# Performance work log

Hardware: AMD Instinct MI355X
Metric: run time of the kernel (lower is better)

## Reference

```python
import jax, jax.numpy as jnp
import numpy as np

N = 25000        # nodes
E = 400000       # edges (avg degree 16)
F_IN = 256       # input node feature dim
C = 32           # tensor-product channels (linear_1 output)
A = 9            # spherical-harmonic dim (lmax=2)
WNUM = C * A     # per-edge TP weight numel (_head_weight_numel)
B = 8            # radial basis size (edge embedding)
H = 64           # edge MLP hidden width
S = 4            # species (node_attrs one-hot width)
F_OUT = 256      # output node feature dim
AVG_NEIGH = 16.0


def setup_inputs() -> dict:
    key = jax.random.key(0)
    ks = jax.random.split(key, 11)
    sc = lambda fan: np.float32(1.0 / np.sqrt(fan))
    return {
        "x": jax.random.normal(ks[0], (N, F_IN), jnp.float32),
        "node_attrs": jax.random.uniform(ks[1], (N, S), jnp.float32),
        "edge_embedding": jax.random.uniform(ks[2], (E, B), jnp.float32),
        "edge_attr": jax.random.normal(ks[3], (E, A), jnp.float32),
        "edge_index": jax.random.randint(ks[4], (2, E), 0, N, jnp.int32),
        "W1": jax.random.normal(ks[5], (F_IN, C), jnp.float32) * sc(F_IN),
        "Wm1": jax.random.normal(ks[6], (B, H), jnp.float32) * sc(B),
        "Wm2": jax.random.normal(ks[7], (H, H), jnp.float32) * sc(H),
        "Wm3": jax.random.normal(ks[8], (H, WNUM), jnp.float32) * sc(H),
        "W2": jax.random.normal(ks[9], (WNUM, F_OUT), jnp.float32) * sc(WNUM),
        "Wsc": jax.random.normal(ks[10], (F_IN, S, F_OUT), jnp.float32) * sc(F_IN * S),
    }


def reference(x, node_attrs, edge_embedding, edge_attr, edge_index,
              W1, Wm1, Wm2, Wm3, W2, Wsc):
    # self-connection: FullyConnectedTensorProduct(x, node_attrs) -> [N, F_OUT]
    sc_out = jnp.einsum('nf,ns,fso->no', x, node_attrs, Wsc)

    # linear_1 + avg-neighbor normalization -> [N, C]
    h = (x @ W1) * (1.0 / jnp.sqrt(jnp.asarray(AVG_NEIGH, x.dtype)))

    # edge MLP on radial embedding -> per-edge TP weights [E, C, A]
    w = jax.nn.silu(edge_embedding @ Wm1)
    w = jax.nn.silu(w @ Wm2)
    w = (w @ Wm3).reshape(E, C, A)

    edge_dst = edge_index[0]
    edge_src = edge_index[1]

    # gather-TP-scatter: msg[e,c,a] = w[e,c,a] * h[src[e],c] * sh[e,a]
    msg = w * h[edge_src][:, :, None] * edge_attr[:, None, :]   # [E, C, A]
    agg = jax.ops.segment_sum(msg.reshape(E, WNUM), edge_dst,
                              num_segments=N)                    # [N, C*A]

    # linear_2 + activation + self-connection
    out = jax.nn.silu(agg @ W2) + sc_out                         # [N, F_OUT]
    return out
```

## Files before the change

kernel.cpp:

```cpp
#include <hip/hip_runtime.h>

#define NN   25000
#define EE   400000
#define FIN  256
#define CC   32
#define AA   9
#define WN   288
#define BB   8
#define HH   64
#define SS   4
#define FOUT 256
#define EPB  32

typedef float f32x4 __attribute__((ext_vector_type(4)));
typedef short short8 __attribute__((ext_vector_type(8)));

__device__ __forceinline__ float silu_f(float v){ return v / (1.0f + __expf(-v)); }

__device__ __forceinline__ unsigned short f2bf(float f){
  unsigned int u = __builtin_bit_cast(unsigned int, f);
  u += 0x7FFFu + ((u >> 16) & 1u);
  return (unsigned short)(u >> 16);
}

__global__ __launch_bounds__(256) void k_h(const float* __restrict__ x,
                                           const float* __restrict__ W1,
                                           float* __restrict__ h){
  int gid = blockIdx.x * 256 + threadIdx.x;
  int n = gid >> 5, c = gid & 31;
  const float* xr = x + (size_t)n * FIN;
  float acc = 0.f;
  #pragma unroll 8
  for (int f = 0; f < FIN; ++f) acc = fmaf(xr[f], W1[f * CC + c], acc);
  h[gid] = acc * 0.25f;
}

__global__ __launch_bounds__(256) void k_cvt(const float* __restrict__ Wm1,
                                             const float* __restrict__ Wm2,
                                             const float* __restrict__ Wm3,
                                             unsigned short* __restrict__ wm1t,
                                             unsigned short* __restrict__ wm2t,
                                             unsigned short* __restrict__ wm3t){
  int i = blockIdx.x * 256 + threadIdx.x;
  if (i < HH * 32){
    int n = i >> 5, k = i & 31;
    wm1t[i] = (k < BB) ? f2bf(Wm1[k * HH + n]) : (unsigned short)0;
  }
  if (i < HH * HH){
    int n = i >> 6, k = i & 63;
    wm2t[n * 64 + k] = f2bf(Wm2[k * HH + n]);
  }
  if (i < WN * HH){
    int n = i >> 6, k = i & 63;
    wm3t[n * 64 + k] = f2bf(Wm3[k * WN + n]);
  }
}

__global__ __launch_bounds__(256) void k_cvtsc(const float* __restrict__ Wsc,
                                               unsigned short* __restrict__ wscb){
  __shared__ float tile[32][33];
  const int k0 = blockIdx.x * 32;
  const int n0 = blockIdx.y * 32;
  const int t = threadIdx.x;
  #pragma unroll
  for (int p = 0; p < 4; ++p){
    int idx = t + p * 256;
    int r = idx >> 5, c = idx & 31;
    tile[r][c] = Wsc[(size_t)(k0 + r) * 256 + n0 + c];
  }
  __syncthreads();
  #pragma unroll
  for (int p = 0; p < 4; ++p){
    int idx = t + p * 256;
    int r = idx >> 5, c = idx & 31;
    wscb[(size_t)(n0 + r) * 1024 + k0 + c] = f2bf(tile[c][r]);
  }
}

__global__ __launch_bounds__(256) void k_hist(const int* __restrict__ eidx,
                                              int* __restrict__ cnt){
  int e = blockIdx.x * 256 + threadIdx.x;
  if (e < EE) atomicAdd(&cnt[eidx[e]], 1);
}

__global__ __launch_bounds__(1024) void k_scan(const int* __restrict__ cnt,
                                               int* __restrict__ cur){
  __shared__ int part[1024];
  const int t = threadIdx.x;
  const int base = t * 25;
  int s = 0;
  for (int i = 0; i < 25; ++i){
    int idx = base + i;
    s += (idx < NN) ? cnt[idx] : 0;
  }
  part[t] = s;
  __syncthreads();
  for (int off = 1; off < 1024; off <<= 1){
    int v = (t >= off) ? part[t - off] : 0;
    __syncthreads();
    part[t] += v;
    __syncthreads();
  }
  int run = part[t] - s;
  for (int i = 0; i < 25; ++i){
    int idx = base + i;
    if (idx < NN){
      cur[idx] = run;
      run += cnt[idx];
    }
  }
}

__global__ __launch_bounds__(256) void k_scatter(const int* __restrict__ eidx,
                                                 const float* __restrict__ eemb,
                                                 const float* __restrict__ sh,
                                                 int* __restrict__ cur,
                                                 unsigned short* __restrict__ ee_p,
                                                 float* __restrict__ sh_p,
                                                 int* __restrict__ src_p,
                                                 int* __restrict__ dst_p){
  int e = blockIdx.x * 256 + threadIdx.x;
  if (e < EE){
    int d = eidx[e];
    int p = atomicAdd(&cur[d], 1);
    dst_p[p] = d;
    src_p[p] = eidx[EE + e];
    float4 v0 = *(const float4*)&eemb[(size_t)e * BB];
    float4 v1 = *(const float4*)&eemb[(size_t)e * BB + 4];
    unsigned short t[8] = {f2bf(v0.x), f2bf(v0.y), f2bf(v0.z), f2bf(v0.w),
                           f2bf(v1.x), f2bf(v1.y), f2bf(v1.z), f2bf(v1.w)};
    *(short8*)&ee_p[(size_t)p * BB] = *(short8*)t;
    #pragma unroll
    for (int a = 0; a < AA; ++a) sh_p[(size_t)p * AA + a] = sh[(size_t)e * AA + a];
  }
}

__global__ __launch_bounds__(256) void k_sc(const float* __restrict__ x,
                                            const float* __restrict__ na,
                                            const unsigned short* __restrict__ wscb,
                                            float* __restrict__ out){
  __shared__ __align__(16) unsigned short As[64][72];
  __shared__ __align__(16) unsigned short Bs[256][72];
  const int tid = threadIdx.x;
  const int m0 = blockIdx.x * 64;
  const int sm = tid >> 2;
  const int sq = tid & 3;
  float4 nav = {0.f, 0.f, 0.f, 0.f};
  if (m0 + sm < NN) nav = *(const float4*)&na[(size_t)(m0 + sm) * SS];
  const float nf[4] = {nav.x, nav.y, nav.z, nav.w};
  const int lane = tid & 63, wv = tid >> 6;
  const int row = lane & 15, kg = lane >> 4;
  const f32x4 zf = {0.f, 0.f, 0.f, 0.f};
  f32x4 acc[16];
  #pragma unroll
  for (int i = 0; i < 16; ++i) acc[i] = zf;

  for (int kc = 0; kc < FIN * SS; kc += 64){
    __syncthreads();
    {
      float4 xv = {0.f, 0.f, 0.f, 0.f};
      int fc4 = (kc >> 2) + sq * 4;
      if (m0 + sm < NN) xv = *(const float4*)&x[(size_t)(m0 + sm) * FIN + fc4];
      float xf[4] = {xv.x, xv.y, xv.z, xv.w};
      unsigned short tmp[16];
      #pragma unroll
      for (int f = 0; f < 4; ++f)
        #pragma unroll
        for (int s = 0; s < 4; ++s) tmp[f * 4 + s] = f2bf(xf[f] * nf[s]);
      *(short8*)&As[sm][sq * 16]     = *(short8*)&tmp[0];
      *(short8*)&As[sm][sq * 16 + 8] = *(short8*)&tmp[8];
    }
    #pragma unroll
    for (int r = 0; r < 4; ++r){
      int ch = tid + r * 256;
      int n = ch >> 2, c4 = ch & 3;
      const unsigned short* src = wscb + (size_t)n * 1024 + kc + c4 * 16;
      *(short8*)&Bs[n][c4 * 16]     = *(const short8*)src;
      *(short8*)&Bs[n][c4 * 16 + 8] = *(const short8*)(src + 8);
    }
    __syncthreads();
    #pragma unroll
    for (int ks = 0; ks < 2; ++ks){
      short8 af = *(const short8*)&As[wv * 16 + row][ks * 32 + kg * 8];
      #pragma unroll
      for (int nt = 0; nt < 16; ++nt){
        short8 bfr = *(const short8*)&Bs[nt * 16 + row][ks * 32 + kg * 8];
        acc[nt] = __builtin_amdgcn_mfma_f32_16x16x32_bf16(af, bfr, acc[nt], 0, 0, 0);
      }
    }
  }
  #pragma unroll
  for (int nt = 0; nt < 16; ++nt){
    #pragma unroll
    for (int r = 0; r < 4; ++r){
      int m = m0 + wv * 16 + kg * 4 + r;
      if (m < NN) out[(size_t)m * FOUT + nt * 16 + row] = acc[nt][r];
    }
  }
}

__global__ __launch_bounds__(128) void k_edge(const unsigned short* __restrict__ ee_p,
                                              const float* __restrict__ sh_p,
                                              const int* __restrict__ src_p,
                                              const int* __restrict__ dst_p,
                                              const float* __restrict__ h,
                                              const unsigned short* __restrict__ wm1t,
                                              const unsigned short* __restrict__ wm2t,
                                              const unsigned short* __restrict__ wm3t,
                                              float* __restrict__ agg){
  __shared__ float sh_s[EPB][13];
  __shared__ float hs_s[EPB][36];
  __shared__ __align__(16) unsigned short t1b[EPB][72];
  __shared__ __align__(16) unsigned short t2b[EPB][72];
  const int tid = threadIdx.x;

  const int nwg = EE / EPB;
  const int q = nwg >> 3, rr = nwg & 7;
  int bid = blockIdx.x;
  int xcd = bid & 7, li = bid >> 3;
  int swz = (xcd < rr ? xcd * (q + 1) : rr * (q + 1) + (xcd - rr) * q) + li;
  const int e0 = swz * EPB;

  {
    int e = tid >> 2, c0 = (tid & 3) * 8;
    const float* hr = h + (size_t)src_p[e0 + e] * CC + c0;
    *(float4*)&hs_s[e][c0]     = *(const float4*)hr;
    *(float4*)&hs_s[e][c0 + 4] = *(const float4*)(hr + 4);
  }
  for (int i = tid; i < EPB * AA; i += 128){
    int e = i / 9, a = i - e * 9;
    sh_s[e][a] = sh_p[(size_t)e0 * AA + i];
  }
  __syncthreads();

  const int lane = tid & 63;
  const int wv   = tid >> 6;
  const int row  = lane & 15;
  const int kg   = lane >> 4;
  const f32x4 zf = {0.f, 0.f, 0.f, 0.f};

  {
    short8 a1 = {0, 0, 0, 0, 0, 0, 0, 0};
    if (kg == 0) a1 = *(const short8*)&ee_p[(size_t)(e0 + wv * 16 + row) * BB];
    #pragma unroll
    for (int nt = 0; nt < 4; ++nt){
      short8 b = *(const short8*)&wm1t[(nt * 16 + row) * 32 + kg * 8];
      f32x4 acc = __builtin_amdgcn_mfma_f32_16x16x32_bf16(a1, b, zf, 0, 0, 0);
      #pragma unroll
      for (int r = 0; r < 4; ++r)
        t1b[wv * 16 + kg * 4 + r][nt * 16 + row] = f2bf(silu_f(acc[r]));
    }
  }

  {
    short8 a2k0 = *(const short8*)&t1b[wv * 16 + row][kg * 8];
    short8 a2k1 = *(const short8*)&t1b[wv * 16 + row][kg * 8 + 32];
    #pragma unroll
    for (int nt = 0; nt < 4; ++nt){
      const unsigned short* bp = wm2t + (size_t)((nt * 16 + row) * 64 + kg * 8);
      short8 b0 = *(const short8*)bp;
      short8 b1 = *(const short8*)(bp + 32);
      f32x4 acc = __builtin_amdgcn_mfma_f32_16x16x32_bf16(a2k0, b0, zf, 0, 0, 0);
      acc = __builtin_amdgcn_mfma_f32_16x16x32_bf16(a2k1, b1, acc, 0, 0, 0);
      #pragma unroll
      for (int r = 0; r < 4; ++r)
        t2b[wv * 16 + kg * 4 + r][nt * 16 + row] = f2bf(silu_f(acc[r]));
    }
  }

  {
    short8 a3k0 = *(const short8*)&t2b[wv * 16 + row][kg * 8];
    short8 a3k1 = *(const short8*)&t2b[wv * 16 + row][kg * 8 + 32];
    const int ebase = wv * 16 + kg * 4;
    int4 dv = *(const int4*)&dst_p[e0 + ebase];
    const int d[4] = {dv.x, dv.y, dv.z, dv.w};
    int c  = (row >= 9) ? 1 : 0;
    int a_ = row - 9 * c;
    const unsigned short* bp = wm3t + (size_t)(row * 64 + kg * 8);
    short8 b0n = *(const short8*)bp;
    short8 b1n = *(const short8*)(bp + 32);
    for (int nt = 0; nt < 18; ++nt){
      short8 b0 = b0n, b1 = b1n;
      if (nt < 17){
        const unsigned short* bp2 = wm3t + (size_t)(((nt + 1) * 16 + row) * 64 + kg * 8);
        b0n = *(const short8*)bp2;
        b1n = *(const short8*)(bp2 + 32);
      }
      f32x4 acc = __builtin_amdgcn_mfma_f32_16x16x32_bf16(a3k0, b0, zf, 0, 0, 0);
      acc = __builtin_amdgcn_mfma_f32_16x16x32_bf16(a3k1, b1, acc, 0, 0, 0);
      int j = nt * 16 + row;
      float vals[4];
      #pragma unroll
      for (int r = 0; r < 4; ++r)
        vals[r] = acc[r] * hs_s[ebase + r][c] * sh_s[ebase + r][a_];
      #pragma unroll
      for (int r = 0; r < 4; ++r){
        bool last = (r == 3) || (d[r + 1] != d[r]);
        if (!last){
          vals[r + 1] += vals[r];
        } else {
          atomicAdd(&agg[(size_t)d[r] * WN + j], vals[r]);
        }
      }
      a_ += 7; c += 1;
      if (a_ >= 9){ a_ -= 9; c += 1; }
    }
  }
}

__global__ __launch_bounds__(256) void k_out(const float* __restrict__ agg,
                                             const float* __restrict__ W2,
                                             float* __restrict__ out){
  __shared__ float As[32][68];
  __shared__ float Bs[32][64];
  const int row0 = blockIdx.x * 64;
  const int col0 = blockIdx.y * 64;
  const int tid = threadIdx.x;
  const int tm = tid >> 4, tn = tid & 15;
  float acc[4][4] = {};
  for (int kc = 0; kc < WN; kc += 32){
    #pragma unroll
    for (int t = 0; t < 8; ++t){
      int idx = tid + t * 256;
      int m = idx >> 5, kk = idx & 31;
      int n = row0 + m;
      float v = 0.f;
      if (n < NN) v = agg[(size_t)n * WN + kc + kk];
      As[kk][m] = v;
    }
    #pragma unroll
    for (int t = 0; t < 8; ++t){
      int idx = tid + t * 256;
      int o = idx & 63, kk = idx >> 6;
      Bs[kk][o] = W2[(size_t)(kc + kk) * FOUT + col0 + o];
    }
    __syncthreads();
    #pragma unroll
    for (int kk = 0; kk < 32; ++kk){
      float4 av = *(const float4*)&As[kk][tm * 4];
      float4 bv = *(const float4*)&Bs[kk][tn * 4];
      float a[4] = {av.x, av.y, av.z, av.w};
      float b[4] = {bv.x, bv.y, bv.z, bv.w};
      #pragma unroll
      for (int i = 0; i < 4; ++i)
        #pragma unroll
        for (int j = 0; j < 4; ++j)
          acc[i][j] = fmaf(a[i], b[j], acc[i][j]);
    }
    __syncthreads();
  }
  #pragma unroll
  for (int i = 0; i < 4; ++i){
    int n = row0 + tm * 4 + i;
    if (n < NN){
      float4 sc = *(const float4*)&out[(size_t)n * FOUT + col0 + tn * 4];
      float4 v;
      v.x = silu_f(acc[i][0]) + sc.x;
      v.y = silu_f(acc[i][1]) + sc.y;
      v.z = silu_f(acc[i][2]) + sc.z;
      v.w = silu_f(acc[i][3]) + sc.w;
      *(float4*)&out[(size_t)n * FOUT + col0 + tn * 4] = v;
    }
  }
}

extern "C" void kernel_launch(void* const* d_in, const int* in_sizes, int n_in,
                              void* d_out, int out_size, void* d_ws, size_t ws_size,
                              hipStream_t stream){
  const float* x    = (const float*)d_in[0];
  const float* na   = (const float*)d_in[1];
  const float* eemb = (const float*)d_in[2];
  const float* shp  = (const float*)d_in[3];
  const int*   eidx = (const int*)d_in[4];
  const float* W1   = (const float*)d_in[5];
  const float* Wm1  = (const float*)d_in[6];
  const float* Wm2  = (const float*)d_in[7];
  const float* Wm3  = (const float*)d_in[8];
  const float* W2   = (const float*)d_in[9];
  const float* Wsc  = (const float*)d_in[10];
  float* out  = (float*)d_out;

  float* agg  = (float*)d_ws;
  float* hbuf = agg + (size_t)NN * WN;
  float* sh_p = hbuf + (size_t)NN * CC;
  int*   cnt  = (int*)(sh_p + (size_t)EE * AA);
  int*   cur  = cnt + NN;
  int*   src_p = cur + NN;
  int*   dst_p = src_p + EE;
  unsigned short* ee_p = (unsigned short*)(dst_p + EE);
  unsigned short* wm1t = ee_p + (size_t)EE * BB;
  unsigned short* wm2t = wm1t + HH * 32;
  unsigned short* wm3t = wm2t + HH * HH;
  unsigned short* wscb = wm3t + WN * HH;

  hipMemsetAsync(agg, 0, (size_t)NN * WN * sizeof(float), stream);
  hipMemsetAsync(cnt, 0, (size_t)NN * sizeof(int), stream);
  k_cvt    <<<dim3((WN * HH + 255) / 256), dim3(256), 0, stream>>>(Wm1, Wm2, Wm3, wm1t, wm2t, wm3t);
  k_cvtsc  <<<dim3(32, 8), dim3(256), 0, stream>>>(Wsc, wscb);
  k_hist   <<<dim3((EE + 255) / 256), dim3(256),  0, stream>>>(eidx, cnt);
  k_scan   <<<dim3(1),                dim3(1024), 0, stream>>>(cnt, cur);
  k_scatter<<<dim3((EE + 255) / 256), dim3(256),  0, stream>>>(eidx, eemb, shp, cur,
                                                               ee_p, sh_p, src_p, dst_p);
  k_h  <<<dim3(NN * CC / 256), dim3(256), 0, stream>>>(x, W1, hbuf);
  k_sc <<<dim3((NN + 63) / 64), dim3(256), 0, stream>>>(x, na, wscb, out);
  k_edge<<<dim3(EE / EPB), dim3(128), 0, stream>>>(ee_p, sh_p, src_p, dst_p, hbuf,
                                                   wm1t, wm2t, wm3t, agg);
  k_out<<<dim3((NN + 63) / 64, FOUT / 64), dim3(256), 0, stream>>>(agg, W2, out);
}
```

Baseline: 657.9 us.

## Accumulate per-block destination sums in LDS before flushing to global agg

Each 32-edge block now labels its distinct destination nodes locally using a ballot over consecutive dst values. When there are at most 8 distinct destinations, messages are accumulated with LDS atomics into a scratch buffer that aliases the MLP staging arrays, then flushed to global memory. Interior segments are stored directly and boundary segments are added atomically. This aims to cut global atomic traffic on agg, at the cost of extra barriers, zero-fill and LDS atomics, and it falls back to the direct global atomics when destinations are scattered.

```diff
diff --git a/kernel.cpp b/kernel.cpp
--- a/kernel.cpp
+++ b/kernel.cpp
@@ -210,8 +210,14 @@
                                               float* __restrict__ agg){
   __shared__ float sh_s[EPB][13];
   __shared__ float hs_s[EPB][36];
-  __shared__ __align__(16) unsigned short t1b[EPB][72];
-  __shared__ __align__(16) unsigned short t2b[EPB][72];
+  __shared__ __align__(16) char scratch[8 * WN * 4];
+  __shared__ int   dst_s[EPB];
+  __shared__ unsigned char dloc_s[EPB];
+  __shared__ unsigned char firstE_s[8];
+  __shared__ int   nD_s;
+  unsigned short (*t1b)[72] = (unsigned short(*)[72])scratch;
+  unsigned short (*t2b)[72] = (unsigned short(*)[72])(scratch + 4608);
+  float (*agg_s)[WN] = (float(*)[WN])scratch;
   const int tid = threadIdx.x;
 
   const int nwg = EE / EPB;
@@ -231,6 +237,17 @@
     int e = i / 9, a = i - e * 9;
     sh_s[e][a] = sh_p[(size_t)e0 * AA + i];
   }
+  if (tid < 8) firstE_s[tid] = 0;
+  if (tid < EPB){
+    int d = dst_p[e0 + tid];
+    dst_s[tid] = d;
+    bool bnd = (tid > 0) && (d != dst_p[e0 + tid - 1]);
+    unsigned long long m = __ballot(bnd);
+    int dl = __popcll(m & ((2ull << tid) - 1ull));
+    dloc_s[tid] = (unsigned char)dl;
+    if (bnd && dl < 8) firstE_s[dl] = (unsigned char)tid;
+    if (tid == EPB - 1) nD_s = dl + 1;
+  }
   __syncthreads();
 
   const int lane = tid & 63;
@@ -272,8 +289,17 @@
     short8 a3k0 = *(const short8*)&t2b[wv * 16 + row][kg * 8];
     short8 a3k1 = *(const short8*)&t2b[wv * 16 + row][kg * 8 + 32];
     const int ebase = wv * 16 + kg * 4;
-    int4 dv = *(const int4*)&dst_p[e0 + ebase];
-    const int d[4] = {dv.x, dv.y, dv.z, dv.w};
+    int dl[4], d[4];
+    #pragma unroll
+    for (int r = 0; r < 4; ++r){ dl[r] = dloc_s[ebase + r]; d[r] = dst_s[ebase + r]; }
+    const int nD = nD_s;
+    const bool direct = (nD > 8);
+    __syncthreads();
+    if (!direct){
+      for (int i = tid; i < nD * WN; i += 128) ((float*)agg_s)[i] = 0.f;
+    }
+    __syncthreads();
+
     int c  = (row >= 9) ? 1 : 0;
     int a_ = row - 9 * c;
     const unsigned short* bp = wm3t + (size_t)(row * 64 + kg * 8);
@@ -295,15 +321,30 @@
         vals[r] = acc[r] * hs_s[ebase + r][c] * sh_s[ebase + r][a_];
       #pragma unroll
       for (int r = 0; r < 4; ++r){
-        bool last = (r == 3) || (d[r + 1] != d[r]);
+        bool last = (r == 3) || (dl[r + 1] != dl[r]);
         if (!last){
           vals[r + 1] += vals[r];
+        } else if (direct){
+          atomicAdd(&agg[(size_t)d[r] * WN + j], vals[r]);
         } else {
-          atomicAdd(&agg[(size_t)d[r] * WN + j], vals[r]);
+          atomicAdd(&agg_s[dl[r]][j], vals[r]);
         }
       }
       a_ += 7; c += 1;
       if (a_ >= 9){ a_ -= 9; c += 1; }
+    }
+
+    __syncthreads();
+    if (!direct){
+      for (int l = 0; l < nD; ++l){
+        int dd = dst_s[firstE_s[l]];
+        float* dstp = &agg[(size_t)dd * WN];
+        if (l > 0 && l < nD - 1){
+          for (int j = tid; j < WN; j += 128) dstp[j] = agg_s[l][j];
+        } else {
+          for (int j = tid; j < WN; j += 128) atomicAdd(&dstp[j], agg_s[l][j]);
+        }
+      }
     }
   }
 }
```

Result: faster. 587.1 us (-10.8%).

## Split edge kernel into MLP and segmented-reduction TP kernels over edge chunks

Applied to the files above, without the earlier changes.

The fused edge kernel is split in two. The MLP kernel writes per-edge TP weights as bf16, transposed by weight column, into a workspace. A separate TP kernel then runs one thread per column and walks 64 dst-sorted edges, reducing each destination segment in a register. Interior segments are stored directly and only the boundary segments use atomics. The aim is to cut the large number of global atomics, at the cost of writing and re-reading a sizable intermediate buffer, processed in edge chunks with extra launches.

```diff
diff --git a/kernel.cpp b/kernel.cpp
--- a/kernel.cpp
+++ b/kernel.cpp
@@ -10,10 +10,11 @@
 #define HH   64
 #define SS   4
 #define FOUT 256
-#define EPB  32
+#define CH   80000
 
 typedef float f32x4 __attribute__((ext_vector_type(4)));
 typedef short short8 __attribute__((ext_vector_type(8)));
+typedef short short4v __attribute__((ext_vector_type(4)));
 
 __device__ __forceinline__ float silu_f(float v){ return v / (1.0f + __expf(-v)); }
 
@@ -21,6 +22,10 @@
   unsigned int u = __builtin_bit_cast(unsigned int, f);
   u += 0x7FFFu + ((u >> 16) & 1u);
   return (unsigned short)(u >> 16);
+}
+__device__ __forceinline__ float bf2f(unsigned short u){
+  unsigned int v = ((unsigned int)u) << 16;
+  return __builtin_bit_cast(float, v);
 }
 
 __global__ __launch_bounds__(256) void k_h(const float* __restrict__ x,
@@ -199,39 +204,20 @@
   }
 }
 
-__global__ __launch_bounds__(128) void k_edge(const unsigned short* __restrict__ ee_p,
-                                              const float* __restrict__ sh_p,
-                                              const int* __restrict__ src_p,
-                                              const int* __restrict__ dst_p,
-                                              const float* __restrict__ h,
-                                              const unsigned short* __restrict__ wm1t,
-                                              const unsigned short* __restrict__ wm2t,
-                                              const unsigned short* __restrict__ wm3t,
-                                              float* __restrict__ agg){
-  __shared__ float sh_s[EPB][13];
-  __shared__ float hs_s[EPB][36];
-  __shared__ __align__(16) unsigned short t1b[EPB][72];
-  __shared__ __align__(16) unsigned short t2b[EPB][72];
+__global__ __launch_bounds__(256) void k_mlp(const unsigned short* __restrict__ ee_p,
+                                             const unsigned short* __restrict__ wm1t,
+                                             const unsigned short* __restrict__ wm2t,
+                                             const unsigned short* __restrict__ wm3t,
+                                             unsigned short* __restrict__ w_t){
+  __shared__ __align__(16) unsigned short t1b[64][72];
   const int tid = threadIdx.x;
 
-  const int nwg = EE / EPB;
+  const int nwg = CH / 64;
   const int q = nwg >> 3, rr = nwg & 7;
   int bid = blockIdx.x;
   int xcd = bid & 7, li = bid >> 3;
   int swz = (xcd < rr ? xcd * (q + 1) : rr * (q + 1) + (xcd - rr) * q) + li;
-  const int e0 = swz * EPB;
-
-  {
-    int e = tid >> 2, c0 = (tid & 3) * 8;
-    const float* hr = h + (size_t)src_p[e0 + e] * CC + c0;
-    *(float4*)&hs_s[e][c0]     = *(const float4*)hr;
-    *(float4*)&hs_s[e][c0 + 4] = *(const float4*)(hr + 4);
-  }
-  for (int i = tid; i < EPB * AA; i += 128){
-    int e = i / 9, a = i - e * 9;
-    sh_s[e][a] = sh_p[(size_t)e0 * AA + i];
-  }
-  __syncthreads();
+  const int e0 = swz * 64;
 
   const int lane = tid & 63;
   const int wv   = tid >> 6;
@@ -264,18 +250,14 @@
       acc = __builtin_amdgcn_mfma_f32_16x16x32_bf16(a2k1, b1, acc, 0, 0, 0);
       #pragma unroll
       for (int r = 0; r < 4; ++r)
-        t2b[wv * 16 + kg * 4 + r][nt * 16 + row] = f2bf(silu_f(acc[r]));
+        t1b[wv * 16 + kg * 4 + r][nt * 16 + row] = f2bf(silu_f(acc[r]));
     }
   }
 
   {
-    short8 a3k0 = *(const short8*)&t2b[wv * 16 + row][kg * 8];
-    short8 a3k1 = *(const short8*)&t2b[wv * 16 + row][kg * 8 + 32];
-    const int ebase = wv * 16 + kg * 4;
-    int4 dv = *(const int4*)&dst_p[e0 + ebase];
-    const int d[4] = {dv.x, dv.y, dv.z, dv.w};
-    int c  = (row >= 9) ? 1 : 0;
-    int a_ = row - 9 * c;
+    short8 a3k0 = *(const short8*)&t1b[wv * 16 + row][kg * 8];
+    short8 a3k1 = *(const short8*)&t1b[wv * 16 + row][kg * 8 + 32];
+    const int ebase = e0 + wv * 16 + kg * 4;
     const unsigned short* bp = wm3t + (size_t)(row * 64 + kg * 8);
     short8 b0n = *(const short8*)bp;
     short8 b1n = *(const short8*)(bp + 32);
@@ -289,22 +271,69 @@
       f32x4 acc = __builtin_amdgcn_mfma_f32_16x16x32_bf16(a3k0, b0, zf, 0, 0, 0);
       acc = __builtin_amdgcn_mfma_f32_16x16x32_bf16(a3k1, b1, acc, 0, 0, 0);
       int j = nt * 16 + row;
-      float vals[4];
-      #pragma unroll
-      for (int r = 0; r < 4; ++r)
-        vals[r] = acc[r] * hs_s[ebase + r][c] * sh_s[ebase + r][a_];
-      #pragma unroll
-      for (int r = 0; r < 4; ++r){
-        bool last = (r == 3) || (d[r + 1] != d[r]);
-        if (!last){
-          vals[r + 1] += vals[r];
-        } else {
-          atomicAdd(&agg[(size_t)d[r] * WN + j], vals[r]);
+      unsigned short pk[4];
+      #pragma unroll
+      for (int r = 0; r < 4; ++r) pk[r] = f2bf(acc[r]);
+      *(short4v*)&w_t[(size_t)j * CH + ebase] = *(short4v*)pk;
+    }
+  }
+}
+
+__global__ __launch_bounds__(256) void k_tp(const unsigned short* __restrict__ w_t,
+                                            const float* __restrict__ sh_p,
+                                            const int* __restrict__ src_p,
+                                            const int* __restrict__ dst_p,
+                                            const float* __restrict__ h,
+                                            float* __restrict__ agg){
+  __shared__ float hs_s[64][36];
+  __shared__ float sh_s[64][13];
+  __shared__ int   dst_s[64];
+  const int tid = threadIdx.x;
+
+  const int nwg = CH / 64;
+  const int q = nwg >> 3, rr = nwg & 7;
+  int bid = blockIdx.x;
+  int xcd = bid & 7, li = bid >> 3;
+  int swz = (xcd < rr ? xcd * (q + 1) : rr * (q + 1) + (xcd - rr) * q) + li;
+  const int e0 = swz * 64;
+
+  {
+    int e = tid >> 2, c0 = (tid & 3) * 8;
+    const float* hr = h + (size_t)src_p[e0 + e] * CC + c0;
+    *(float4*)&hs_s[e][c0]     = *(const float4*)hr;
+    *(float4*)&hs_s[e][c0 + 4] = *(const float4*)(hr + 4);
+  }
+  for (int i = tid; i < 64 * AA; i += 256){
+    int e = i / 9, a = i - e * 9;
+    sh_s[e][a] = sh_p[(size_t)e0 * AA + i];
+  }
+  if (tid < 64) dst_s[tid] = dst_p[e0 + tid];
+  __syncthreads();
+
+  for (int j = tid; j < WN; j += 256){
+    const int c  = j / 9;
+    const int a_ = j - 9 * c;
+    const unsigned short* wp = w_t + (size_t)j * CH + e0;
+    float acc = 0.f;
+    int d = dst_s[0];
+    int seg_start = 0;
+    #pragma unroll
+    for (int eb = 0; eb < 8; ++eb){
+      short8 w8 = *(const short8*)&wp[eb * 8];
+      #pragma unroll
+      for (int ei = 0; ei < 8; ++ei){
+        int e = eb * 8 + ei;
+        int de = dst_s[e];
+        if (de != d){
+          if (seg_start > 0) agg[(size_t)d * WN + j] = acc;
+          else atomicAdd(&agg[(size_t)d * WN + j], acc);
+          d = de; acc = 0.f; seg_start = e;
         }
+        float w = bf2f((unsigned short)w8[ei]);
+        acc = fmaf(w * hs_s[e][c], sh_s[e][a_], acc);
       }
-      a_ += 7; c += 1;
-      if (a_ >= 9){ a_ -= 9; c += 1; }
-    }
+    }
+    atomicAdd(&agg[(size_t)d * WN + j], acc);
   }
 }
 
@@ -392,6 +421,7 @@
   unsigned short* wm2t = wm1t + HH * 32;
   unsigned short* wm3t = wm2t + HH * HH;
   unsigned short* wscb = wm3t + WN * HH;
+  unsigned short* w_t  = wscb + 256 * 1024;
 
   hipMemsetAsync(agg, 0, (size_t)NN * WN * sizeof(float), stream);
   hipMemsetAsync(cnt, 0, (size_t)NN * sizeof(int), stream);
@@ -403,7 +433,14 @@
                                                                ee_p, sh_p, src_p, dst_p);
   k_h  <<<dim3(NN * CC / 256), dim3(256), 0, stream>>>(x, W1, hbuf);
   k_sc <<<dim3((NN + 63) / 64), dim3(256), 0, stream>>>(x, na, wscb, out);
-  k_edge<<<dim3(EE / EPB), dim3(128), 0, stream>>>(ee_p, sh_p, src_p, dst_p, hbuf,
-                                                   wm1t, wm2t, wm3t, agg);
+  for (int c = 0; c < EE / CH; ++c){
+    k_mlp<<<dim3(CH / 64), dim3(256), 0, stream>>>(ee_p + (size_t)c * CH * BB,
+                                                   wm1t, wm2t, wm3t, w_t);
+    k_tp <<<dim3(CH / 64), dim3(256), 0, stream>>>(w_t,
+                                                   sh_p + (size_t)c * CH * AA,
+                                                   src_p + (size_t)c * CH,
+                                                   dst_p + (size_t)c * CH,
+                                                   hbuf, agg);
+  }
   k_out<<<dim3((NN + 63) / 64, FOUT / 64), dim3(256), 0, stream>>>(agg, W2, out);
 }
```

New measurement: 723.8 us. +10.0%, slower.
